# Performance work log

Measured on AMD Instinct MI355X. Metric: run time of the kernel, lower is better.

The kernel has to match this reference:

```python
import jax, jax.numpy as jnp
import numpy as np

NUM_BINS = 20
TEMPERATURE = 0.1
EPS = 1e-8


def setup_inputs() -> dict:
    key = jax.random.key(0)
    k1, k2 = jax.random.split(key)
    shape = (32, 1, 1024, 1024)  # B, C, H, W segmentation-style probability maps
    preds = jax.random.uniform(k1, shape, dtype=jnp.float32)
    targets = jax.random.uniform(k2, shape, dtype=jnp.float32)
    return {"preds": preds, "targets": targets}


def reference(preds, targets):
    p = preds.reshape(-1)
    t = targets.reshape(-1)
    centers = jnp.linspace(0.0, 1.0, NUM_BINS, dtype=p.dtype)

    def per_bin(c):
        # Gaussian soft-assignment weights for this bin center
        w = jnp.exp(-(p - c) ** 2 / TEMPERATURE)
        w_sum = w.sum()
        e = (w * p).sum() / (w_sum + EPS)  # weighted mean confidence
        o = (w * t).sum() / (w_sum + EPS)  # weighted mean accuracy
        # torch code skips bins with zero total weight
        return jnp.where(w_sum == 0.0, jnp.zeros_like(e), jnp.abs(e - o))

    # lax.map loops sequentially over the 20 bin centers so we never
    # materialize a [NUM_BINS, N] weight matrix.
    contribs = jax.lax.map(per_bin, centers)
    return contribs.sum() / NUM_BINS
```

## Files before the change

### kernel.cpp

```cpp
#include <hip/hip_runtime.h>
#include <math.h>
#include <stdint.h>

#define NUM_BINS 20
#define NPAIR    (NUM_BINS / 2)
#define NACC     (3 * NUM_BINS)
#define BLOCK    256
#define NBLK     1024
#define TILEF    (BLOCK * 4)

typedef float v2f __attribute__((ext_vector_type(2)));
typedef __attribute__((address_space(3))) uint32_t       lds_u32_t;
typedef __attribute__((address_space(1))) const uint32_t glb_u32_t;

__device__ __host__ constexpr float K1f() { return (float)(-1.0 / (0.1 * 0.6931471805599453)); }
__device__ __host__ constexpr float K2f() { return (float)( 2.0 / (1.9 * 0.6931471805599453)); }

__device__ __forceinline__ void stage16(const float4* gsrc, float* ldst) {
    __builtin_amdgcn_global_load_lds((glb_u32_t*)gsrc, (lds_u32_t*)ldst, 16, 0, 0);
}

__global__ __launch_bounds__(BLOCK, 4) void ace_partial(const float* __restrict__ p,
                                                        const float* __restrict__ t,
                                                        float* __restrict__ partials,
                                                        int n4, int nblk) {
    __shared__ float ldsP[2][TILEF];
    __shared__ float ldsT[2][TILEF];

    const float K1 = K1f();
    const float K2 = K2f();

    v2f aW2[NPAIR], aP2[NPAIR], aT2[NPAIR];
#pragma unroll
    for (int jp = 0; jp < NPAIR; ++jp) {
        aW2[jp] = (v2f){0.f, 0.f};
        aP2[jp] = (v2f){0.f, 0.f};
        aT2[jp] = (v2f){0.f, 0.f};
    }

    const float4* __restrict__ p4 = (const float4*)p;
    const float4* __restrict__ t4 = (const float4*)t;

    const int tid    = threadIdx.x;
    const int wave   = tid >> 6;
    const int stride = gridDim.x * BLOCK;
    int gidx         = blockIdx.x * BLOCK + tid;
    const int niter  = n4 / stride;

    float* const ldsPbase = &ldsP[0][0];
    float* const ldsTbase = &ldsT[0][0];
    const int waveOff = wave * 256;

    int cur = 0;
    if (niter > 0) {
        stage16(p4 + gidx, ldsPbase + waveOff);
        stage16(t4 + gidx, ldsTbase + waveOff);
        asm volatile("s_waitcnt vmcnt(0)" ::: "memory");
        __syncthreads();
    }

    for (int k = 0; k < niter; ++k) {
        const int gnext = gidx + stride;
        if (k + 1 < niter) {
            const int nb = cur ^ 1;
            stage16(p4 + gnext, ldsPbase + nb * TILEF + waveOff);
            stage16(t4 + gnext, ldsTbase + nb * TILEF + waveOff);
        }

        const float4 pv = *(const float4*)(ldsPbase + cur * TILEF + tid * 4);
        const float4 tv = *(const float4*)(ldsTbase + cur * TILEF + tid * 4);

        float pe[4] = {pv.x, pv.y, pv.z, pv.w};
        float te[4] = {tv.x, tv.y, tv.z, tv.w};

#pragma unroll
        for (int e = 0; e < 4; ++e) {
            float pp = pe[e];
            float tt = te[e];
            float u  = __builtin_amdgcn_exp2f(K1 * pp * pp);
            float G  = __builtin_amdgcn_exp2f(K2 * pp);
            float GG = G * G;
            v2f g2;  g2.x = u;  g2.y = u * G;
            v2f GG2 = (v2f){GG, GG};
            v2f pp2 = (v2f){pp, pp};
            v2f tt2 = (v2f){tt, tt};
#pragma unroll
            for (int jp = 0; jp < NPAIR; ++jp) {
                aW2[jp] += g2;
                aP2[jp]  = __builtin_elementwise_fma(g2, pp2, aP2[jp]);
                aT2[jp]  = __builtin_elementwise_fma(g2, tt2, aT2[jp]);
                g2      *= GG2;
            }
        }

        __syncthreads();
        cur ^= 1;
        gidx = gnext;
    }

    for (int i = gidx; i < n4; i += stride) {
        float4 pv = p4[i];
        float4 tv = t4[i];
        float pe[4] = {pv.x, pv.y, pv.z, pv.w};
        float te[4] = {tv.x, tv.y, tv.z, tv.w};
#pragma unroll
        for (int e = 0; e < 4; ++e) {
            float pp = pe[e];
            float tt = te[e];
            float u  = __builtin_amdgcn_exp2f(K1 * pp * pp);
            float G  = __builtin_amdgcn_exp2f(K2 * pp);
            float GG = G * G;
            v2f g2;  g2.x = u;  g2.y = u * G;
            v2f GG2 = (v2f){GG, GG};
            v2f pp2 = (v2f){pp, pp};
            v2f tt2 = (v2f){tt, tt};
#pragma unroll
            for (int jp = 0; jp < NPAIR; ++jp) {
                aW2[jp] += g2;
                aP2[jp]  = __builtin_elementwise_fma(g2, pp2, aP2[jp]);
                aT2[jp]  = __builtin_elementwise_fma(g2, tt2, aT2[jp]);
                g2      *= GG2;
            }
        }
    }

#pragma unroll
    for (int jp = 0; jp < NPAIR; ++jp) {
#pragma unroll
        for (int off = 32; off > 0; off >>= 1) {
            aW2[jp].x += __shfl_down(aW2[jp].x, off, 64);
            aW2[jp].y += __shfl_down(aW2[jp].y, off, 64);
            aP2[jp].x += __shfl_down(aP2[jp].x, off, 64);
            aP2[jp].y += __shfl_down(aP2[jp].y, off, 64);
            aT2[jp].x += __shfl_down(aT2[jp].x, off, 64);
            aT2[jp].y += __shfl_down(aT2[jp].y, off, 64);
        }
    }

    __shared__ float red[BLOCK / 64][NACC];
    int lane = threadIdx.x & 63;
    if (lane == 0) {
#pragma unroll
        for (int jp = 0; jp < NPAIR; ++jp) {
            red[wave][2 * jp]                    = aW2[jp].x;
            red[wave][2 * jp + 1]                = aW2[jp].y;
            red[wave][NUM_BINS + 2 * jp]         = aP2[jp].x;
            red[wave][NUM_BINS + 2 * jp + 1]     = aP2[jp].y;
            red[wave][2 * NUM_BINS + 2 * jp]     = aT2[jp].x;
            red[wave][2 * NUM_BINS + 2 * jp + 1] = aT2[jp].y;
        }
    }
    __syncthreads();

    if (threadIdx.x < NACC) {
        float s = 0.f;
#pragma unroll
        for (int w = 0; w < BLOCK / 64; ++w) s += red[w][threadIdx.x];
        partials[threadIdx.x * nblk + blockIdx.x] = s;
    }
}

__global__ __launch_bounds__(1024) void ace_final(const float* __restrict__ partials,
                                                  float* __restrict__ out,
                                                  int nblk) {
    const float K1 = K1f();

    __shared__ float red[NACC][16];
    __shared__ float sums[NACC];
    int tid = threadIdx.x;

    if (tid < NACC * 16) {
        int j = tid >> 4;
        int k = tid & 15;
        float s = 0.f;
        for (int b = k; b < nblk; b += 16) s += partials[j * nblk + b];
        red[j][k] = s;
    }
    __syncthreads();

    if (tid < NACC) {
        float s = 0.f;
#pragma unroll
        for (int k = 0; k < 16; ++k) s += red[tid][k];
        sums[tid] = s;
    }
    __syncthreads();

    if (tid == 0) {
        float acc = 0.f;
        for (int j = 0; j < NUM_BINS; ++j) {
            float c    = (float)j / 19.0f;
            float A    = __builtin_amdgcn_exp2f(K1 * c * c);
            float wsum = A * sums[j];
            float denom = wsum + 1e-8f;
            float e    = (A * sums[NUM_BINS + j]) / denom;
            float o    = (A * sums[2 * NUM_BINS + j]) / denom;
            float contrib = (wsum == 0.0f) ? 0.0f : fabsf(e - o);
            acc += contrib;
        }
        out[0] = acc / (float)NUM_BINS;
    }
}

extern "C" void kernel_launch(void* const* d_in, const int* in_sizes, int n_in,
                              void* d_out, int out_size, void* d_ws, size_t ws_size,
                              hipStream_t stream) {
    const float* preds   = (const float*)d_in[0];
    const float* targets = (const float*)d_in[1];
    float* out           = (float*)d_out;
    float* partials      = (float*)d_ws;

    int n  = in_sizes[0];
    int n4 = n >> 2;

    int nblk = NBLK;
    size_t need = (size_t)nblk * NACC * sizeof(float);
    if (ws_size < need) {
        nblk = (int)(ws_size / (NACC * sizeof(float)));
        if (nblk < 1) nblk = 1;
    }

    ace_partial<<<nblk, BLOCK, 0, stream>>>(preds, targets, partials, n4, nblk);
    ace_final<<<1, 1024, 0, stream>>>(partials, out, nblk);
}
```

Before: 301.9 us.

## Use per-wave 4-deep LDS prefetch ring and drop block-wide barriers

Replaces the block-wide double-buffered LDS staging with a per-wave ring of four slots. Each wave prefetches three tiles ahead and waits with explicit vmcnt counts instead of __syncthreads. This deepens memory-level parallelism and removes barrier stalls in the streaming loop, at the cost of more LDS per block, which may limit occupancy. The final reduction also reads partials as float4.

```diff
diff --git a/kernel.cpp b/kernel.cpp
--- a/kernel.cpp
+++ b/kernel.cpp
@@ -7,7 +7,9 @@
 #define NACC     (3 * NUM_BINS)
 #define BLOCK    256
 #define NBLK     1024
-#define TILEF    (BLOCK * 4)
+#define DEPTH    4
+#define CHUNKF   256
+#define NWAVES   (BLOCK / 64)
 
 typedef float v2f __attribute__((ext_vector_type(2)));
 typedef __attribute__((address_space(3))) uint32_t       lds_u32_t;
@@ -19,13 +21,16 @@
 __device__ __forceinline__ void stage16(const float4* gsrc, float* ldst) {
     __builtin_amdgcn_global_load_lds((glb_u32_t*)gsrc, (lds_u32_t*)ldst, 16, 0, 0);
 }
+
+#define WAIT_VMCNT(n) asm volatile("s_waitcnt vmcnt(" #n ")" ::: "memory")
+#define WAIT_LGKM0()  asm volatile("s_waitcnt lgkmcnt(0)" ::: "memory")
 
 __global__ __launch_bounds__(BLOCK, 4) void ace_partial(const float* __restrict__ p,
                                                         const float* __restrict__ t,
                                                         float* __restrict__ partials,
                                                         int n4, int nblk) {
-    __shared__ float ldsP[2][TILEF];
-    __shared__ float ldsT[2][TILEF];
+    __shared__ float ldsP[NWAVES][DEPTH][CHUNKF];
+    __shared__ float ldsT[NWAVES][DEPTH][CHUNKF];
 
     const float K1 = K1f();
     const float K2 = K2f();
@@ -43,32 +48,33 @@
 
     const int tid    = threadIdx.x;
     const int wave   = tid >> 6;
+    const int lane   = tid & 63;
     const int stride = gridDim.x * BLOCK;
-    int gidx         = blockIdx.x * BLOCK + tid;
+    const int base   = blockIdx.x * BLOCK + tid;
     const int niter  = n4 / stride;
 
-    float* const ldsPbase = &ldsP[0][0];
-    float* const ldsTbase = &ldsT[0][0];
-    const int waveOff = wave * 256;
-
-    int cur = 0;
-    if (niter > 0) {
-        stage16(p4 + gidx, ldsPbase + waveOff);
-        stage16(t4 + gidx, ldsTbase + waveOff);
-        asm volatile("s_waitcnt vmcnt(0)" ::: "memory");
-        __syncthreads();
+    const int npre = (niter < DEPTH - 1) ? niter : (DEPTH - 1);
+    for (int k = 0; k < npre; ++k) {
+        stage16(p4 + base + k * stride, &ldsP[wave][k][0]);
+        stage16(t4 + base + k * stride, &ldsT[wave][k][0]);
     }
 
     for (int k = 0; k < niter; ++k) {
-        const int gnext = gidx + stride;
-        if (k + 1 < niter) {
-            const int nb = cur ^ 1;
-            stage16(p4 + gnext, ldsPbase + nb * TILEF + waveOff);
-            stage16(t4 + gnext, ldsTbase + nb * TILEF + waveOff);
-        }
-
-        const float4 pv = *(const float4*)(ldsPbase + cur * TILEF + tid * 4);
-        const float4 tv = *(const float4*)(ldsTbase + cur * TILEF + tid * 4);
+        const int rem = niter - 1 - k;
+        if (rem >= 2)      { WAIT_VMCNT(4); }
+        else if (rem == 1) { WAIT_VMCNT(2); }
+        else               { WAIT_VMCNT(0); }
+
+        const int slot = k & (DEPTH - 1);
+        const float4 pv = *(const float4*)&ldsP[wave][slot][lane * 4];
+        const float4 tv = *(const float4*)&ldsT[wave][slot][lane * 4];
+        WAIT_LGKM0();
+
+        if (k + DEPTH - 1 < niter) {
+            const int kn = k + DEPTH - 1;
+            stage16(p4 + base + kn * stride, &ldsP[wave][kn & (DEPTH - 1)][0]);
+            stage16(t4 + base + kn * stride, &ldsT[wave][kn & (DEPTH - 1)][0]);
+        }
 
         float pe[4] = {pv.x, pv.y, pv.z, pv.w};
         float te[4] = {tv.x, tv.y, tv.z, tv.w};
@@ -92,13 +98,9 @@
                 g2      *= GG2;
             }
         }
-
-        __syncthreads();
-        cur ^= 1;
-        gidx = gnext;
-    }
-
-    for (int i = gidx; i < n4; i += stride) {
+    }
+
+    for (int i = base + niter * stride; i < n4; i += stride) {
         float4 pv = p4[i];
         float4 tv = t4[i];
         float pe[4] = {pv.x, pv.y, pv.z, pv.w};
@@ -137,8 +139,7 @@
         }
     }
 
-    __shared__ float red[BLOCK / 64][NACC];
-    int lane = threadIdx.x & 63;
+    __shared__ float red[NWAVES][NACC];
     if (lane == 0) {
 #pragma unroll
         for (int jp = 0; jp < NPAIR; ++jp) {
@@ -155,7 +156,7 @@
     if (threadIdx.x < NACC) {
         float s = 0.f;
 #pragma unroll
-        for (int w = 0; w < BLOCK / 64; ++w) s += red[w][threadIdx.x];
+        for (int w = 0; w < NWAVES; ++w) s += red[w][threadIdx.x];
         partials[threadIdx.x * nblk + blockIdx.x] = s;
     }
 }
@@ -172,8 +173,14 @@
     if (tid < NACC * 16) {
         int j = tid >> 4;
         int k = tid & 15;
+        const float4* row4 = (const float4*)(partials + (size_t)j * nblk);
+        int n4b = nblk >> 2;
         float s = 0.f;
-        for (int b = k; b < nblk; b += 16) s += partials[j * nblk + b];
+        for (int b = k; b < n4b; b += 16) {
+            float4 v = row4[b];
+            s += (v.x + v.y) + (v.z + v.w);
+        }
+        for (int b = (n4b << 2) + k; b < nblk; b += 16) s += partials[(size_t)j * nblk + b];
         red[j][k] = s;
     }
     __syncthreads();
```

Result: faster. 294.7 us (-2.4%).
